# Optimization experiments

Measured on AMD Instinct MI355X. Metric: run time of the kernel, lower is better.

The kernel has to match this reference:

```python
import jax, jax.numpy as jnp
import numpy as np

B, C, H, W = 4, 256, 224, 224
WH = WW = 8
SH = SW = 4
HEADS = 8
HD = C // HEADS
N = WH * WW
EPS = 1e-5


def _rel_index():
    coords = np.stack(np.meshgrid(np.arange(WH), np.arange(WW), indexing='ij')).reshape(2, -1)
    rel = (coords[:, :, None] - coords[:, None, :]).transpose(1, 2, 0).copy()
    rel[:, :, 0] += WH - 1
    rel[:, :, 1] += WW - 1
    rel[:, :, 0] *= 2 * WW - 1
    return rel.sum(-1)  # (N, N) int

REL_INDEX = _rel_index()


def _shift_mask(Hp, Wp):
    # Swin shift mask for one image: (nW, N, N) float, 0 or -100
    img = np.zeros((Hp, Wp))
    cnt = 0
    for a, b in [(0, Hp - WH), (Hp - WH, Hp - SH), (Hp - SH, Hp)]:
        for c, d in [(0, Wp - WW), (Wp - WW, Wp - SW), (Wp - SW, Wp)]:
            img[a:b, c:d] = cnt
            cnt += 1
    mw = img.reshape(Hp // WH, WH, Wp // WW, WW).transpose(0, 2, 1, 3).reshape(-1, N)
    diff = mw[:, None, :] - mw[:, :, None]  # [w, i, j] = mw[w,j] - mw[w,i]
    return np.where(diff != 0, np.float32(-100.0), np.float32(0.0)).astype(np.float32)


def _ln(x, w, b):
    m = jnp.mean(x, axis=-1, keepdims=True)
    v = jnp.mean(jnp.square(x - m), axis=-1, keepdims=True)
    return (x - m) * jax.lax.rsqrt(v + EPS) * w + b


def setup_inputs() -> dict:
    key = jax.random.key(0)
    ks = jax.random.split(key, 8)
    num_rel = (2 * WH - 1) * (2 * WW - 1)
    return {
        'x': jax.random.normal(ks[0], (B, C, H, W), dtype=jnp.float32),
        'qkv_w': jax.random.normal(ks[1], (3 * C, C), dtype=jnp.float32) * 0.02,
        'proj_w': jax.random.normal(ks[2], (C, C), dtype=jnp.float32) * 0.02,
        'proj_b': jnp.zeros((C,), dtype=jnp.float32),
        'rpb_table': jax.random.normal(ks[3], (num_rel, HEADS), dtype=jnp.float32) * 0.02,
        'norm1_w': jnp.ones((C,), dtype=jnp.float32),
        'norm1_b': jnp.zeros((C,), dtype=jnp.float32),
        'norm2_w': jnp.ones((C,), dtype=jnp.float32),
        'norm2_b': jnp.zeros((C,), dtype=jnp.float32),
        'mlp_w1': jax.random.normal(ks[4], (4 * C, C), dtype=jnp.float32) * 0.02,
        'mlp_b1': jnp.zeros((4 * C,), dtype=jnp.float32),
        'mlp_w2': jax.random.normal(ks[5], (C, 4 * C), dtype=jnp.float32) * 0.02,
        'mlp_b2': jnp.zeros((C,), dtype=jnp.float32),
    }


def reference(x, qkv_w, proj_w, proj_b, rpb_table, norm1_w, norm1_b,
              norm2_w, norm2_b, mlp_w1, mlp_b1, mlp_w2, mlp_b2):
    Bx, Cx, Hx, Wx = x.shape
    pad_h = (WH - Hx % WH) % WH
    pad_w = (WW - Wx % WW) % WW
    if pad_h or pad_w:
        x = jnp.pad(x, ((0, 0), (0, 0), (0, pad_h), (0, pad_w)))
    Hp, Wp = Hx + pad_h, Wx + pad_w
    x = jnp.transpose(x, (0, 2, 3, 1))                    # BHWC
    x = jnp.roll(x, (-SH, -SW), axis=(1, 2))
    nW = (Hp // WH) * (Wp // WW)
    # window partition -> (B*nW, N, C), batch-major
    xw = x.reshape(Bx, Hp // WH, WH, Wp // WW, WW, Cx)
    xw = jnp.transpose(xw, (0, 1, 3, 2, 4, 5)).reshape(-1, N, Cx)

    # ----- windowed attention -----
    h = _ln(xw, norm1_w, norm1_b)
    qkv = (h @ qkv_w.T).reshape(-1, N, 3, HEADS, HD)
    qkv = jnp.transpose(qkv, (2, 0, 3, 1, 4))             # (3, Bw, heads, N, hd)
    q, k, v = qkv[0], qkv[1], qkv[2]
    attn = jnp.einsum('bhnd,bhmd->bhnm', q, k) * (1.0 / HD ** 0.5)
    bias = jnp.transpose(rpb_table[REL_INDEX.reshape(-1)].reshape(N, N, HEADS), (2, 0, 1))
    attn = attn + bias[None]
    # faithful to torch: repeat_interleave(B, dim=0) -> window-major mask ordering
    mask = jnp.asarray(_shift_mask(Hp, Wp))               # (nW, N, N)
    attn = attn + jnp.repeat(mask, Bx, axis=0)[:, None]
    attn = jax.nn.softmax(attn, axis=-1)
    out = jnp.einsum('bhnm,bhmd->bhnd', attn, v)
    out = jnp.transpose(out, (0, 2, 1, 3)).reshape(-1, N, Cx)
    out = out @ proj_w.T + proj_b
    xw = xw + out

    # ----- MLP -----
    h = _ln(xw, norm2_w, norm2_b)
    h = jax.nn.gelu(h @ mlp_w1.T + mlp_b1, approximate=False) @ mlp_w2.T + mlp_b2
    xw = xw + h

    # window reverse, un-shift, un-pad
    x = xw.reshape(Bx, Hp // WH, Wp // WW, WH, WW, Cx)
    x = jnp.transpose(x, (0, 1, 3, 2, 4, 5)).reshape(Bx, Hp, Wp, Cx)
    x = jnp.roll(x, (SH, SW), axis=(1, 2))
    x = x[:, :Hx, :Wx, :]
    return jnp.transpose(x, (0, 3, 1, 2))
```

## Files before the change

### kernel.cpp

```cpp
#include <hip/hip_runtime.h>

typedef unsigned short u16;
typedef unsigned int   u32;
typedef __attribute__((ext_vector_type(8))) __bf16 bf16x8;
typedef __attribute__((ext_vector_type(4))) float  f32x4;
typedef __attribute__((ext_vector_type(4))) u16    u16x4;
typedef __attribute__((ext_vector_type(8))) u16    u16x8;

#define DEV __device__ __forceinline__

DEV u16 f2b(float f) {
  union { float f; u32 u; } a; a.f = f;
  const u32 u = a.u;
  return (u16)((u + 0x7fffu + ((u >> 16) & 1u)) >> 16);
}

DEV float gelu_fast(float x) {
  const float x2 = x * x;
  const float t  = __builtin_fmaf(0.1029430f, x2, 2.3022150f);
  const float e  = __builtin_exp2f(x * t);
  const float r  = __builtin_amdgcn_rcpf(1.0f + e);
  return __builtin_fmaf(-x, r, x);
}

DEV void gload16(const void* g, void* l) {
  __builtin_amdgcn_global_load_lds(
      (const __attribute__((address_space(1))) void*)g,
      (__attribute__((address_space(3))) void*)l, 16, 0, 0);
}

__global__ __launch_bounds__(256)
void conv_weights(const float* __restrict__ qkvw, const float* __restrict__ projw,
                  const float* __restrict__ w1,   const float* __restrict__ w2,
                  u16* __restrict__ dq, u16* __restrict__ dp,
                  u16* __restrict__ d1, u16* __restrict__ d2) {
  const int t = blockIdx.x * 256 + threadIdx.x;
  if (t < 196608)      dq[t]          = f2b(qkvw[t]);
  else if (t < 262144) dp[t - 196608] = f2b(projw[t - 196608]);
  else if (t < 524288) d1[t - 262144] = f2b(w1[t - 262144]);
  else                 d2[t - 524288] = f2b(w2[t - 524288]);
}

__global__ __launch_bounds__(256)
void ln1_win(const float* __restrict__ x, const float* __restrict__ w1,
             const float* __restrict__ b1, u16* __restrict__ hout,
             float* __restrict__ xwout) {
  __shared__ float xt[64 * 257];
  __shared__ float smean[256], srstd[256];
  const int tid = threadIdx.x, lane = tid & 63, wv = tid >> 6;
  const int g = blockIdx.x;
  const int b = g / 196, rem = g % 196;
  const int wh = rem / 7, wg = rem % 7;
  const int base_r = b * 784 + wh * 28 + wg * 4;
  const int pr = tid >> 5, pc = tid & 31;
  int hp = wh * 8 + 4 + pr; if (hp >= 224) hp -= 224;
  int wp = wg * 32 + 4 + pc; if (wp >= 224) wp -= 224;
  const long roff = (long)b * 256 * 50176 + hp * 224 + wp;

  float s = 0.f, q = 0.f;
  for (int cc = 0; cc < 4; ++cc) {
#pragma unroll 8
    for (int i = 0; i < 64; ++i) {
      const int c = cc * 64 + i;
      const float v = x[(long)c * 50176 + roff];
      xt[i * 257 + tid] = v;
      s += v; q += v * v;
    }
    __syncthreads();
#pragma unroll 8
    for (int jj = 0; jj < 64; ++jj) {
      const int p = jj * 4 + wv;
      const int m = (base_r + ((p & 31) >> 3)) * 64 + (p >> 5) * 8 + (p & 7);
      xwout[(long)m * 256 + cc * 64 + lane] = xt[lane * 257 + p];
    }
    __syncthreads();
  }
  const float mean = s * (1.f / 256.f);
  smean[tid] = mean;
  srstd[tid] = rsqrtf(q * (1.f / 256.f) - mean * mean + 1e-5f);
  __syncthreads();

  float wr_[4], br_[4];
#pragma unroll
  for (int cc = 0; cc < 4; ++cc) { wr_[cc] = w1[cc * 64 + lane]; br_[cc] = b1[cc * 64 + lane]; }
#pragma unroll 2
  for (int jj = 0; jj < 64; ++jj) {
    const int p = jj * 4 + wv;
    const int m = (base_r + ((p & 31) >> 3)) * 64 + (p >> 5) * 8 + (p & 7);
    const float mu = smean[p], rs = srstd[p];
#pragma unroll
    for (int cc = 0; cc < 4; ++cc) {
      const float v = xwout[(long)m * 256 + cc * 64 + lane];
      hout[(long)m * 256 + cc * 64 + lane] = f2b((v - mu) * rs * wr_[cc] + br_[cc]);
    }
  }
}

template<int EPI, int NCOL>
__global__ __launch_bounds__(512, 2)
void gemm_bt(const u16* __restrict__ A, const u16* __restrict__ Bw, const int K,
             float* __restrict__ fout, const float* __restrict__ bias,
             u16* __restrict__ bout,
             const float* __restrict__ lnw, const float* __restrict__ lnb) {
  __shared__ __align__(16) u16 smem[65536];
  u16* sA0 = smem;
  u16* sB0 = smem + 16384;
  u16* sA1 = smem + 32768;
  u16* sB1 = smem + 49152;

  const int tid  = threadIdx.x;
  const int lane = tid & 63;
  const int wid  = tid >> 6;
  const int wr   = wid >> 2;
  const int wc   = wid & 3;

  const int nwg = gridDim.x;
  const int bid = blockIdx.x;
  const int wg  = (bid & 7) * (nwg >> 3) + (bid >> 3);
  const int row_blk = wg / NCOL;
  const int col_blk = wg - row_blk * NCOL;
  const int row0 = row_blk * 256;
  const int col0 = (EPI == 5) ? 512 : col_blk * 256;

  const f32x4 vzero = {0.f, 0.f, 0.f, 0.f};
  f32x4 acc[8][4];
#pragma unroll
  for (int i = 0; i < 8; ++i)
#pragma unroll
    for (int j = 0; j < 4; ++j) acc[i][j] = vzero;

  const int lrow = lane >> 3;
  const int lcol = ((lane & 7) << 3) ^ (lane & 56);
  const int l15  = lane & 15;
  const int l4   = lane >> 4;
  const int ksw  = (lane & 7) << 3;

  const u16* pA = A  + (long)(row0 + lrow) * K + lcol;
  const u16* pB = Bw + (long)(col0 + lrow) * K + lcol;

#define STAGE_TILE(KT, DA, DB)                                       \
  {                                                                  \
    _Pragma("unroll")                                                \
    for (int ch = 0; ch < 4; ++ch) {                                 \
      const int rr = ch * 64 + wid * 8;                              \
      gload16(pA + (long)rr * K + (KT), (DA) + rr * 64);             \
      gload16(pB + (long)rr * K + (KT), (DB) + rr * 64);             \
    }                                                                \
  }

#define COMPUTE_TILE(SA, SB)                                                            \
  {                                                                                     \
    _Pragma("unroll")                                                                   \
    for (int kk = 0; kk < 2; ++kk) {                                                    \
      bf16x8 af[8], bfv[4];                                                             \
      _Pragma("unroll")                                                                 \
      for (int mi = 0; mi < 8; ++mi)                                                    \
        af[mi] = *(const bf16x8*)((SA) + (wr * 128 + mi * 16 + l15) * 64 +              \
                                  ((kk * 32 + l4 * 8) ^ ksw));                          \
      _Pragma("unroll")                                                                 \
      for (int nj = 0; nj < 4; ++nj)                                                    \
        bfv[nj] = *(const bf16x8*)((SB) + (wc * 64 + nj * 16 + l15) * 64 +              \
                                   ((kk * 32 + l4 * 8) ^ ksw));                         \
      _Pragma("unroll")                                                                 \
      for (int mi = 0; mi < 8; ++mi)                                                    \
        _Pragma("unroll")                                                               \
        for (int nj = 0; nj < 4; ++nj) {                                                \
          if (EPI == 5)                                                                 \
            acc[mi][nj] = __builtin_amdgcn_mfma_f32_16x16x32_bf16(af[mi], bfv[nj],      \
                                                                  acc[mi][nj], 0, 0, 0);\
          else                                                                          \
            acc[mi][nj] = __builtin_amdgcn_mfma_f32_16x16x32_bf16(bfv[nj], af[mi],      \
                                                                  acc[mi][nj], 0, 0, 0);\
        }                                                                               \
    }                                                                                   \
  }

  const int nt = K >> 6;
  STAGE_TILE(0, sA0, sB0);
  __syncthreads();
  for (int t = 0; t < nt; t += 2) {
    if (t + 1 < nt) STAGE_TILE((t + 1) << 6, sA1, sB1);
    COMPUTE_TILE(sA0, sB0);
    __syncthreads();
    if (t + 1 < nt) {
      if (t + 2 < nt) STAGE_TILE((t + 2) << 6, sA0, sB0);
      COMPUTE_TILE(sA1, sB1);
      __syncthreads();
    }
  }
#undef STAGE_TILE
#undef COMPUTE_TILE

  if (EPI == 0) {
#pragma unroll
    for (int mi = 0; mi < 8; ++mi) {
      const int m = row0 + wr * 128 + mi * 16 + l15;
      const int rr = m >> 6, ii = m & 63;
#pragma unroll
      for (int nj = 0; nj < 4; ++nj) {
        const int n = col0 + wc * 64 + nj * 16 + (l4 << 2);
        const int s = n >> 8, hh = (n >> 5) & 7, d = n & 31;
        u16x4 p;
#pragma unroll
        for (int reg = 0; reg < 4; ++reg) p[reg] = f2b(acc[mi][nj][reg]);
        *(u16x4*)(bout + (long)s * 51380224L +
                  (long)((rr * 8 + hh) * 64 + ii) * 32 + d) = p;
      }
    }
  } else if (EPI == 5) {
#pragma unroll
    for (int mi = 0; mi < 8; ++mi) {
      const int mb = row0 + wr * 128 + mi * 16 + (l4 << 2);
      const int rrg = mb >> 6, ii = mb & 63;
#pragma unroll
      for (int nj = 0; nj < 4; ++nj) {
        const int n = 512 + wc * 64 + nj * 16 + l15;
        const int hh = (n >> 5) & 7, d = n & 31;
        u16x4 p;
#pragma unroll
        for (int reg = 0; reg < 4; ++reg) p[reg] = f2b(acc[mi][nj][reg]);
        *(u16x4*)(bout + 102760448L + (long)((rrg * 8 + hh) * 32 + d) * 64 + ii) = p;
      }
    }
  } else if (EPI == 1) {
    f32x4 b4[4];
#pragma unroll
    for (int nj = 0; nj < 4; ++nj)
      b4[nj] = *(const f32x4*)(bias + wc * 64 + nj * 16 + (l4 << 2));
    float sS[8], sQ[8];
#pragma unroll
    for (int mi = 0; mi < 8; ++mi) {
      const int m = row0 + wr * 128 + mi * 16 + l15;
      float* yrow = fout + (long)m * 256;
      float s = 0.f, q = 0.f;
#pragma unroll
      for (int nj = 0; nj < 4; ++nj) {
        const int n = wc * 64 + nj * 16 + (l4 << 2);
        f32x4 o = *(f32x4*)(yrow + n);
#pragma unroll
        for (int reg = 0; reg < 4; ++reg) {
          o[reg] += acc[mi][nj][reg] + b4[nj][reg];
          s += o[reg]; q += o[reg] * o[reg];
        }
        *(f32x4*)(yrow + n) = o;
        acc[mi][nj] = o;
      }
      s += __shfl_xor(s, 16); s += __shfl_xor(s, 32);
      q += __shfl_xor(q, 16); q += __shfl_xor(q, 32);
      sS[mi] = s; sQ[mi] = q;
    }
    float* ps = (float*)smem;
    float* pq = ps + 1024;
    if (lane < 16) {
#pragma unroll
      for (int mi = 0; mi < 8; ++mi) {
        const int idx = ((wr * 8 + mi) * 16 + l15) * 4 + wc;
        ps[idx] = sS[mi]; pq[idx] = sQ[mi];
      }
    }
    __syncthreads();
#pragma unroll
    for (int mi = 0; mi < 8; ++mi) {
      const int m = row0 + wr * 128 + mi * 16 + l15;
      const int base = ((wr * 8 + mi) * 16 + l15) * 4;
      const float S = ps[base] + ps[base + 1] + ps[base + 2] + ps[base + 3];
      const float Q = pq[base] + pq[base + 1] + pq[base + 2] + pq[base + 3];
      const float mean = S * (1.f / 256.f);
      const float rstd = rsqrtf(Q * (1.f / 256.f) - mean * mean + 1e-5f);
#pragma unroll
      for (int nj = 0; nj < 4; ++nj) {
        const int n = wc * 64 + nj * 16 + (l4 << 2);
        const f32x4 w4 = *(const f32x4*)(lnw + n);
        const f32x4 c4 = *(const f32x4*)(lnb + n);
        u16x4 p;
#pragma unroll
        for (int reg = 0; reg < 4; ++reg)
          p[reg] = f2b((acc[mi][nj][reg] - mean) * rstd * w4[reg] + c4[reg]);
        *(u16x4*)(bout + (long)m * 256 + n) = p;
      }
    }
  } else if (EPI == 3) {
    f32x4 b4[4];
#pragma unroll
    for (int nj = 0; nj < 4; ++nj)
      b4[nj] = *(const f32x4*)(bias + wc * 64 + nj * 16 + (l4 << 2));
#pragma unroll
    for (int mi = 0; mi < 8; ++mi) {
      const int m = row0 + wr * 128 + mi * 16 + l15;
      float* yrow = fout + (long)m * 256;
#pragma unroll
      for (int nj = 0; nj < 4; ++nj) {
        const int n = wc * 64 + nj * 16 + (l4 << 2);
        f32x4 o = *(f32x4*)(yrow + n);
#pragma unroll
        for (int reg = 0; reg < 4; ++reg) o[reg] += acc[mi][nj][reg] + b4[nj][reg];
        *(f32x4*)(yrow + n) = o;
      }
    }
  } else {
    f32x4 b4[4];
#pragma unroll
    for (int nj = 0; nj < 4; ++nj)
      b4[nj] = *(const f32x4*)(bias + col0 + wc * 64 + nj * 16 + (l4 << 2));
#pragma unroll
    for (int mi = 0; mi < 8; ++mi) {
      const int m = row0 + wr * 128 + mi * 16 + l15;
#pragma unroll
      for (int nj = 0; nj < 4; ++nj) {
        const int n = col0 + wc * 64 + nj * 16 + (l4 << 2);
        u16x4 p;
#pragma unroll
        for (int reg = 0; reg < 4; ++reg)
          p[reg] = f2b(gelu_fast(acc[mi][nj][reg] + b4[nj][reg]));
        *(u16x4*)(bout + (long)m * 1024 + n) = p;
      }
    }
  }
}

__global__ __launch_bounds__(256)
void attn_win(const u16* __restrict__ qkv, const float* __restrict__ rpb,
              u16* __restrict__ aout) {
  __shared__ u16 Pl[4][4096];
  __shared__ float srpb[1800];
  const int tid = threadIdx.x, lane = tid & 63, wv = tid >> 6;
  const int bid = blockIdx.x;
  const int r = bid >> 1;
  const int h = (bid & 1) * 4 + wv;
  for (int i = tid; i < 1800; i += 256) srpb[i] = rpb[i];
  __syncthreads();

  const int midx = r >> 2;
  const int wh = midx / 28, ww = midx % 28;
  const int l15 = lane & 15, l4 = lane >> 4;

  u16* Pw = &Pl[wv][0];
  const long hb = (long)(r * 8 + h) * 2048;
  const u16* qh = qkv + hb;
  const u16* kh = qkv + 51380224 + hb;
  const u16* vh = qkv + 102760448 + hb;

  int rj[4], cj[4], labj[4];
#pragma unroll
  for (int nj = 0; nj < 4; ++nj) {
    const int j = nj * 16 + l15;
    rj[nj] = j >> 3; cj[nj] = j & 7;
    const int hp = wh * 8 + rj[nj], wp = ww * 8 + cj[nj];
    const int lh = (hp < 216) ? 0 : ((hp < 220) ? 1 : 2);
    const int lw = (wp < 216) ? 0 : ((wp < 220) ? 1 : 2);
    labj[nj] = lh * 3 + lw;
  }

  const f32x4 vzero = {0.f, 0.f, 0.f, 0.f};

  bf16x8 qf[4], kf[4];
#pragma unroll
  for (int mi = 0; mi < 4; ++mi)
    qf[mi] = *(const bf16x8*)(qh + (mi * 16 + l15) * 32 + l4 * 8);
#pragma unroll
  for (int nj = 0; nj < 4; ++nj)
    kf[nj] = *(const bf16x8*)(kh + (nj * 16 + l15) * 32 + l4 * 8);

  f32x4 S[4][4];
#pragma unroll
  for (int mi = 0; mi < 4; ++mi)
#pragma unroll
    for (int nj = 0; nj < 4; ++nj)
      S[mi][nj] = __builtin_amdgcn_mfma_f32_16x16x32_bf16(qf[mi], kf[nj], vzero, 0, 0, 0);

#pragma unroll
  for (int mi = 0; mi < 4; ++mi)
#pragma unroll
    for (int reg = 0; reg < 4; ++reg) {
      const int i = mi * 16 + (l4 << 2) + reg;
      const int ri = i >> 3, ci = i & 7;
      const int hp = wh * 8 + ri, wp = ww * 8 + ci;
      const int lh = (hp < 216) ? 0 : ((hp < 220) ? 1 : 2);
      const int lw = (wp < 216) ? 0 : ((wp < 220) ? 1 : 2);
      const int li = lh * 3 + lw;
      float v[4];
#pragma unroll
      for (int nj = 0; nj < 4; ++nj) {
        const int idx = (ri - rj[nj] + 7) * 15 + (ci - cj[nj] + 7);
        v[nj] = S[mi][nj][reg] * 0.17677669529663687f + srpb[idx * 8 + h]
              + ((li != labj[nj]) ? -100.0f : 0.0f);
      }
      float mx = fmaxf(fmaxf(v[0], v[1]), fmaxf(v[2], v[3]));
      mx = fmaxf(mx, __shfl_xor(mx, 1));
      mx = fmaxf(mx, __shfl_xor(mx, 2));
      mx = fmaxf(mx, __shfl_xor(mx, 4));
      mx = fmaxf(mx, __shfl_xor(mx, 8));
      float sum = 0.f;
#pragma unroll
      for (int nj = 0; nj < 4; ++nj) { v[nj] = __expf(v[nj] - mx); sum += v[nj]; }
      sum += __shfl_xor(sum, 1);
      sum += __shfl_xor(sum, 2);
      sum += __shfl_xor(sum, 4);
      sum += __shfl_xor(sum, 8);
      const float rinv = __builtin_amdgcn_rcpf(sum);
      const int sw = (i & 7) << 3;
#pragma unroll
      for (int nj = 0; nj < 4; ++nj)
        Pw[i * 64 + ((nj * 16 + l15) ^ sw)] = f2b(v[nj] * rinv);
    }

  f32x4 OT[2][4];
#pragma unroll
  for (int td = 0; td < 2; ++td)
#pragma unroll
    for (int ti = 0; ti < 4; ++ti) OT[td][ti] = vzero;

  const int rsw = (l15 & 7) << 3;
#pragma unroll
  for (int kk = 0; kk < 2; ++kk) {
    bf16x8 pf[4], vf[2];
#pragma unroll
    for (int ti = 0; ti < 4; ++ti)
      pf[ti] = *(const bf16x8*)(Pw + (ti * 16 + l15) * 64 + ((kk * 32 + l4 * 8) ^ rsw));
#pragma unroll
    for (int td = 0; td < 2; ++td)
      vf[td] = *(const bf16x8*)(vh + (td * 16 + l15) * 64 + kk * 32 + l4 * 8);
#pragma unroll
    for (int td = 0; td < 2; ++td)
#pragma unroll
      for (int ti = 0; ti < 4; ++ti)
        OT[td][ti] = __builtin_amdgcn_mfma_f32_16x16x32_bf16(vf[td], pf[ti], OT[td][ti], 0, 0, 0);
  }

#pragma unroll
  for (int td = 0; td < 2; ++td)
#pragma unroll
    for (int ti = 0; ti < 4; ++ti) {
      const int i = ti * 16 + l15;
      const int d0 = td * 16 + (l4 << 2);
      u16x4 p;
#pragma unroll
      for (int reg = 0; reg < 4; ++reg) p[reg] = f2b(OT[td][ti][reg]);
      *(u16x4*)(aout + (long)(r * 64 + i) * 256 + h * 32 + d0) = p;
    }
}

__global__ __launch_bounds__(256)
void unwin(const float* __restrict__ y, float* __restrict__ out) {
  __shared__ float xt[64 * 257];
  const int tid = threadIdx.x, lane = tid & 63, wv = tid >> 6;
  const int g = blockIdx.x;
  const int b = g / 196, rem = g % 196;
  const int wh = rem / 7, wg = rem % 7;
  const int base_r = b * 784 + wh * 28 + wg * 4;
  const int pr = tid >> 5, pc = tid & 31;
  int hp = wh * 8 + 4 + pr; if (hp >= 224) hp -= 224;
  int wp = wg * 32 + 4 + pc; if (wp >= 224) wp -= 224;
  const long woff = (long)b * 256 * 50176 + hp * 224 + wp;

  for (int cc = 0; cc < 4; ++cc) {
#pragma unroll 8
    for (int jj = 0; jj < 64; ++jj) {
      const int p = jj * 4 + wv;
      const int m = (base_r + ((p & 31) >> 3)) * 64 + (p >> 5) * 8 + (p & 7);
      xt[lane * 257 + p] = y[(long)m * 256 + cc * 64 + lane];
    }
    __syncthreads();
#pragma unroll 8
    for (int i = 0; i < 64; ++i)
      out[(long)(cc * 64 + i) * 50176 + woff] = xt[i * 257 + tid];
    __syncthreads();
  }
}

extern "C" void kernel_launch(void* const* d_in, const int* in_sizes, int n_in,
                              void* d_out, int out_size, void* d_ws, size_t ws_size,
                              hipStream_t stream) {
  (void)in_sizes; (void)n_in; (void)out_size; (void)ws_size;
  const float* x     = (const float*)d_in[0];
  const float* qkvw  = (const float*)d_in[1];
  const float* projw = (const float*)d_in[2];
  const float* projb = (const float*)d_in[3];
  const float* rpb   = (const float*)d_in[4];
  const float* n1w   = (const float*)d_in[5];
  const float* n1b   = (const float*)d_in[6];
  const float* n2w   = (const float*)d_in[7];
  const float* n2b   = (const float*)d_in[8];
  const float* w1    = (const float*)d_in[9];
  const float* b1    = (const float*)d_in[10];
  const float* w2    = (const float*)d_in[11];
  const float* b2    = (const float*)d_in[12];

  char* ws = (char*)d_ws;
  u16*   hbuf   = (u16*)(ws);
  u16*   qkvb   = (u16*)(ws + 102760448);
  u16*   abuf   = (u16*)(ws + 411041792);
  float* ybuf   = (float*)(ws + 513802240);
  u16*   hidb   = (u16*)(ws + 102760448);
  u16*   qkvwb  = (u16*)(ws + 719323136);
  u16*   projwb = (u16*)(ws + 719716352);
  u16*   w1b    = (u16*)(ws + 719847424);
  u16*   w2b    = (u16*)(ws + 720371712);

  conv_weights<<<3072, 256, 0, stream>>>(qkvw, projw, w1, w2, qkvwb, projwb, w1b, w2b);
  ln1_win<<<784, 256, 0, stream>>>(x, n1w, n1b, hbuf, ybuf);
  gemm_bt<0, 2><<<1568, 512, 0, stream>>>(hbuf, qkvwb, 256, nullptr, nullptr, qkvb, nullptr, nullptr);
  gemm_bt<5, 1><<<784, 512, 0, stream>>>(hbuf, qkvwb, 256, nullptr, nullptr, qkvb, nullptr, nullptr);
  attn_win<<<6272, 256, 0, stream>>>(qkvb, rpb, abuf);
  gemm_bt<1, 1><<<784, 512, 0, stream>>>(abuf, projwb, 256, ybuf, projb, hbuf, n2w, n2b);
  gemm_bt<2, 4><<<3136, 512, 0, stream>>>(hbuf, w1b, 256, nullptr, b1, hidb, nullptr, nullptr);
  gemm_bt<3, 1><<<784, 512, 0, stream>>>(hidb, w2b, 1024, ybuf, b2, nullptr, nullptr, nullptr);
  unwin<<<784, 256, 0, stream>>>(ybuf, (float*)d_out);
}
```

Before: 1.257 ms.

## Merge QKV GEMM launches and overlap tile prefetch with fine-grained waitcnt

The two QKV GEMM launches (Q/K tiles and the transposed V tile) become one launch of 2352 blocks, where column block 2 takes the V-transposed epilogue path. The K loop is rewritten as a single double-buffered loop. It uses explicit s_waitcnt vmcnt(8) and raw s_barrier so the next tile's global loads stay in flight while the current tile is computed. This removes one kernel launch and tail, and aims to hide more load latency. An extra __syncthreads is added in the LN epilogue because LDS is now reused without a trailing full sync, and the MFMA operand order is flipped for non-swapped paths.

```diff
diff --git a/kernel.cpp b/kernel.cpp
--- a/kernel.cpp
+++ b/kernel.cpp
@@ -120,7 +120,7 @@
   const int row_blk = wg / NCOL;
   const int col_blk = wg - row_blk * NCOL;
   const int row0 = row_blk * 256;
-  const int col0 = (EPI == 5) ? 512 : col_blk * 256;
+  const int col0 = col_blk * 256;
 
   const f32x4 vzero = {0.f, 0.f, 0.f, 0.f};
   f32x4 acc[8][4];
@@ -148,7 +148,7 @@
     }                                                                \
   }
 
-#define COMPUTE_TILE(SA, SB)                                                            \
+#define COMPUTE_TILE(SA, SB, SWAP)                                                      \
   {                                                                                     \
     _Pragma("unroll")                                                                   \
     for (int kk = 0; kk < 2; ++kk) {                                                    \
@@ -165,31 +165,65 @@
       for (int mi = 0; mi < 8; ++mi)                                                    \
         _Pragma("unroll")                                                               \
         for (int nj = 0; nj < 4; ++nj) {                                                \
-          if (EPI == 5)                                                                 \
-            acc[mi][nj] = __builtin_amdgcn_mfma_f32_16x16x32_bf16(af[mi], bfv[nj],      \
+          if (SWAP)                                                                     \
+            acc[mi][nj] = __builtin_amdgcn_mfma_f32_16x16x32_bf16(bfv[nj], af[mi],      \
                                                                   acc[mi][nj], 0, 0, 0);\
           else                                                                          \
-            acc[mi][nj] = __builtin_amdgcn_mfma_f32_16x16x32_bf16(bfv[nj], af[mi],      \
+            acc[mi][nj] = __builtin_amdgcn_mfma_f32_16x16x32_bf16(af[mi], bfv[nj],      \
                                                                   acc[mi][nj], 0, 0, 0);\
         }                                                                               \
     }                                                                                   \
   }
 
-  const int nt = K >> 6;
-  STAGE_TILE(0, sA0, sB0);
-  __syncthreads();
-  for (int t = 0; t < nt; t += 2) {
-    if (t + 1 < nt) STAGE_TILE((t + 1) << 6, sA1, sB1);
-    COMPUTE_TILE(sA0, sB0);
-    __syncthreads();
-    if (t + 1 < nt) {
-      if (t + 2 < nt) STAGE_TILE((t + 2) << 6, sA0, sB0);
-      COMPUTE_TILE(sA1, sB1);
-      __syncthreads();
-    }
-  }
+#define KLOOP(SWAP)                                                  \
+  {                                                                  \
+    const int nt = K >> 6;                                           \
+    STAGE_TILE(0, sA0, sB0);                                         \
+    int cur = 0;                                                     \
+    for (int t = 0; t < nt; ++t) {                                   \
+      u16* cA = cur ? sA1 : sA0;                                     \
+      u16* cB = cur ? sB1 : sB0;                                     \
+      u16* nA = cur ? sA0 : sA1;                                     \
+      u16* nB = cur ? sB0 : sB1;                                     \
+      if (t + 1 < nt) {                                              \
+        STAGE_TILE((t + 1) << 6, nA, nB);                            \
+        asm volatile("s_waitcnt vmcnt(8)" ::: "memory");             \
+      } else {                                                       \
+        asm volatile("s_waitcnt vmcnt(0)" ::: "memory");             \
+      }                                                              \
+      __builtin_amdgcn_s_barrier();                                  \
+      asm volatile("" ::: "memory");                                 \
+      COMPUTE_TILE(cA, cB, SWAP);                                    \
+      asm volatile("" ::: "memory");                                 \
+      __builtin_amdgcn_s_barrier();                                  \
+      cur ^= 1;                                                      \
+    }                                                                \
+  }
+
+  if (EPI == 0 && col_blk == 2) {
+    KLOOP(0);
+#pragma unroll
+    for (int mi = 0; mi < 8; ++mi) {
+      const int mb = row0 + wr * 128 + mi * 16 + (l4 << 2);
+      const int rrg = mb >> 6, ii = mb & 63;
+#pragma unroll
+      for (int nj = 0; nj < 4; ++nj) {
+        const int n = 512 + wc * 64 + nj * 16 + l15;
+        const int hh = (n >> 5) & 7, d = n & 31;
+        u16x4 p;
+#pragma unroll
+        for (int reg = 0; reg < 4; ++reg) p[reg] = f2b(acc[mi][nj][reg]);
+        *(u16x4*)(bout + 102760448L + (long)((rrg * 8 + hh) * 32 + d) * 64 + ii) = p;
+      }
+    }
+    return;
+  }
+
+  KLOOP(1);
+
 #undef STAGE_TILE
 #undef COMPUTE_TILE
+#undef KLOOP
 
   if (EPI == 0) {
 #pragma unroll
@@ -205,21 +239,6 @@
         for (int reg = 0; reg < 4; ++reg) p[reg] = f2b(acc[mi][nj][reg]);
         *(u16x4*)(bout + (long)s * 51380224L +
                   (long)((rr * 8 + hh) * 64 + ii) * 32 + d) = p;
-      }
-    }
-  } else if (EPI == 5) {
-#pragma unroll
-    for (int mi = 0; mi < 8; ++mi) {
-      const int mb = row0 + wr * 128 + mi * 16 + (l4 << 2);
-      const int rrg = mb >> 6, ii = mb & 63;
-#pragma unroll
-      for (int nj = 0; nj < 4; ++nj) {
-        const int n = 512 + wc * 64 + nj * 16 + l15;
-        const int hh = (n >> 5) & 7, d = n & 31;
-        u16x4 p;
-#pragma unroll
-        for (int reg = 0; reg < 4; ++reg) p[reg] = f2b(acc[mi][nj][reg]);
-        *(u16x4*)(bout + 102760448L + (long)((rrg * 8 + hh) * 32 + d) * 64 + ii) = p;
       }
     }
   } else if (EPI == 1) {
@@ -251,6 +270,7 @@
     }
     float* ps = (float*)smem;
     float* pq = ps + 1024;
+    __syncthreads();
     if (lane < 16) {
 #pragma unroll
       for (int mi = 0; mi < 8; ++mi) {
@@ -297,7 +317,7 @@
         *(f32x4*)(yrow + n) = o;
       }
     }
-  } else {
+  } else if (EPI == 2) {
     f32x4 b4[4];
 #pragma unroll
     for (int nj = 0; nj < 4; ++nj)
@@ -499,8 +519,7 @@
 
   conv_weights<<<3072, 256, 0, stream>>>(qkvw, projw, w1, w2, qkvwb, projwb, w1b, w2b);
   ln1_win<<<784, 256, 0, stream>>>(x, n1w, n1b, hbuf, ybuf);
-  gemm_bt<0, 2><<<1568, 512, 0, stream>>>(hbuf, qkvwb, 256, nullptr, nullptr, qkvb, nullptr, nullptr);
-  gemm_bt<5, 1><<<784, 512, 0, stream>>>(hbuf, qkvwb, 256, nullptr, nullptr, qkvb, nullptr, nullptr);
+  gemm_bt<0, 3><<<2352, 512, 0, stream>>>(hbuf, qkvwb, 256, nullptr, nullptr, qkvb, nullptr, nullptr);
   attn_win<<<6272, 256, 0, stream>>>(qkvb, rpb, abuf);
   gemm_bt<1, 1><<<784, 512, 0, stream>>>(abuf, projwb, 256, ybuf, projb, hbuf, n2w, n2b);
   gemm_bt<2, 4><<<3136, 512, 0, stream>>>(hbuf, w1b, 256, nullptr, b1, hidb, nullptr, nullptr);
```

Result: no change. 1.244 ms (-1.0%).
